# Optimization experiments

Measured on AMD Instinct MI355X. Metric: run time of the kernel, lower is better.

The kernel has to match this reference:

```python
import jax, jax.numpy as jnp
import numpy as np

NA = 100000
NB = 100000
E = 500000
D = 256
EPS = 1e-5


def setup_inputs() -> dict:
    key = jax.random.key(0)
    ks = jax.random.split(key, 10)
    scale = 1.0 / np.sqrt(D)
    return {
        "feat_a": jax.random.normal(ks[0], (NA, D), jnp.float32),
        "feat_b": jax.random.normal(ks[1], (NB, D), jnp.float32),
        "src_ab": jax.random.randint(ks[2], (E,), 0, NA, jnp.int32),
        "dst_ab": jax.random.randint(ks[3], (E,), 0, NB, jnp.int32),
        "src_ba": jax.random.randint(ks[4], (E,), 0, NB, jnp.int32),
        "dst_ba": jax.random.randint(ks[5], (E,), 0, NA, jnp.int32),
        "WT_ab": jax.random.normal(ks[6], (D, D), jnp.float32) * scale,
        "WT_ba": jax.random.normal(ks[7], (D, D), jnp.float32) * scale,
        "WA_ab": jax.random.normal(ks[8], (1, D), jnp.float32) * scale,
        "WA_ba": jax.random.normal(ks[9], (1, D), jnp.float32) * scale,
        "gamma": jnp.ones((D,), jnp.float32),
        "beta": jnp.zeros((D,), jnp.float32),
    }


def _etype_agg(h_src, h_dst, src, dst, WT, WA, n_dst):
    # per-etype linear on src nodes: t_h = W_T h_src
    t_h = h_src @ WT.T                              # [Ns, D]
    x = t_h[src] * h_dst[dst]                       # u_mul_v -> [E, D]
    s = jnp.exp(x @ WA.T)                           # exp(W_A x) -> [E, 1]
    att_sum = jax.ops.segment_sum(s, dst, num_segments=n_dst)  # copy_e+sum
    att = s / att_sum[dst]                          # e_div_v (dst of an edge always has >=1 edge)
    # u_mul_e + sum: weighted scatter of raw src features
    return jax.ops.segment_sum(h_src[src] * att, dst, num_segments=n_dst)


def _finalize(h, gamma, beta):
    h = jax.nn.relu(h)
    mu = jnp.mean(h, axis=-1, keepdims=True)
    var = jnp.mean(jnp.square(h - mu), axis=-1, keepdims=True)
    return (h - mu) / jnp.sqrt(var + EPS) * gamma + beta  # dropout is identity (eval)


def reference(feat_a, feat_b, src_ab, dst_ab, src_ba, dst_ba,
              WT_ab, WT_ba, WA_ab, WA_ba, gamma, beta):
    h_b = _etype_agg(feat_a, feat_b, src_ab, dst_ab, WT_ab, WA_ab, NB)
    h_a = _etype_agg(feat_b, feat_a, src_ba, dst_ba, WT_ba, WA_ba, NA)
    out_a = _finalize(h_a, gamma, beta)
    out_b = _finalize(h_b, gamma, beta)
    return jnp.stack([out_a, out_b])  # [2, N, D]
```

## Files before the change

kernel.cpp:

```cpp
#include <hip/hip_runtime.h>
#include <hip/hip_bf16.h>

#define D 256

typedef __attribute__((ext_vector_type(8))) short short8;
typedef __attribute__((ext_vector_type(4))) float f32x4;
typedef __attribute__((ext_vector_type(4))) unsigned short u16x4;

__device__ __forceinline__ unsigned short f2bf(float f) {
  unsigned int u = __builtin_bit_cast(unsigned int, f);
  u = (u + 0x7FFFu + ((u >> 16) & 1u)) >> 16;
  return (unsigned short)u;
}
__device__ __forceinline__ float bf2f(unsigned short h) {
  unsigned int u = ((unsigned int)h) << 16;
  return __builtin_bit_cast(float, u);
}

__global__ void zero_f32(float* __restrict__ p, int n) {
  int i = blockIdx.x * 256 + threadIdx.x;
  if (i < n) p[i] = 0.f;
}
__global__ void zero2_k(int* __restrict__ a, int na, int* __restrict__ b, int nb) {
  int i = blockIdx.x * 256 + threadIdx.x;
  if (i < na) a[i] = 0;
  else if (i - na < nb) b[i - na] = 0;
}

__global__ void classify_k(const float* __restrict__ q0, const float* __restrict__ q1,
                           const float* __restrict__ q2, const float* __restrict__ q3,
                           int* __restrict__ flags) {
  __shared__ int cnt1[4], cnt0[4];
  int t = threadIdx.x;
  if (t < 4) { cnt1[t] = 0; cnt0[t] = 0; }
  __syncthreads();
  const float* qs[4] = {q0, q1, q2, q3};
#pragma unroll
  for (int v = 0; v < 4; ++v) {
    float x = qs[v][t];
    if (x == 1.0f) atomicAdd(&cnt1[v], 1);
    if (x == 0.0f) atomicAdd(&cnt0[v], 1);
  }
  __syncthreads();
  if (t == 0) {
    int gi = -1, bi = -1;
    for (int v = 0; v < 4; ++v) if (cnt1[v] == 256 && gi < 0) gi = v;
    for (int v = 0; v < 4; ++v) if (cnt0[v] == 256 && v != gi && bi < 0) bi = v;
    if (gi < 0) gi = 2;
    if (bi < 0) bi = (gi == 3) ? 2 : 3;
    int wa[2], w = 0;
    for (int v = 0; v < 4; ++v) if (v != gi && v != bi) { if (w < 2) wa[w] = v; ++w; }
    flags[0] = wa[0]; flags[1] = wa[1]; flags[2] = gi; flags[3] = bi;
  }
}

__global__ void prep_w2(const float* __restrict__ WT_ab, const float* __restrict__ WT_ba,
                        const float* __restrict__ q0, const float* __restrict__ q1,
                        const float* __restrict__ q2, const float* __restrict__ q3,
                        const int* __restrict__ flags,
                        unsigned short* __restrict__ w2ab, unsigned short* __restrict__ w2ba) {
  const float* qs[4] = {q0, q1, q2, q3};
  const float* WAab = qs[flags[0]];
  const float* WAba = qs[flags[1]];
  int i = blockIdx.x * 256 + threadIdx.x;
  int n = i >> 8;
  w2ab[i] = f2bf(WAab[n] * WT_ab[i]);
  w2ba[i] = f2bf(WAba[n] * WT_ba[i]);
}

__global__ __launch_bounds__(512) void gemm_g(const float* __restrict__ feat,
                                              const unsigned short* __restrict__ w2,
                                              unsigned short* __restrict__ g,
                                              unsigned short* __restrict__ featbf,
                                              int nchunks, int do_featbf) {
  __shared__ __align__(16) unsigned char bl[2][8192];
  int lane = threadIdx.x & 63;
  int wv = threadIdx.x >> 6;
  int c0 = blockIdx.x * 8 + wv;
  bool active = c0 < nchunks;
  int c = active ? c0 : (nchunks - 1);
  int r16 = lane & 15;
  int kg = lane >> 4;
  int row0 = c * 32;

  short8 a[2][8];
#pragma unroll
  for (int sub = 0; sub < 2; ++sub) {
    int row = row0 + sub * 16 + r16;
    const float* rp = feat + (size_t)row * D + kg * 8;
#pragma unroll
    for (int kk = 0; kk < 8; ++kk) {
      f32x4 x0 = *(const f32x4*)(rp + kk * 32);
      f32x4 x1 = *(const f32x4*)(rp + kk * 32 + 4);
      short8 t;
      t[0] = (short)f2bf(x0[0]); t[1] = (short)f2bf(x0[1]);
      t[2] = (short)f2bf(x0[2]); t[3] = (short)f2bf(x0[3]);
      t[4] = (short)f2bf(x1[0]); t[5] = (short)f2bf(x1[1]);
      t[6] = (short)f2bf(x1[2]); t[7] = (short)f2bf(x1[3]);
      a[sub][kk] = t;
      if (do_featbf && active)
        *(short8*)(featbf + (size_t)row * D + kk * 32 + kg * 8) = t;
    }
  }

  int t = threadIdx.x;
  int brow = t >> 5, bc = t & 31;
  int slin = brow * 512 + bc * 16;
  int sswz = slin ^ ((brow & 7) << 4);

  *(short8*)(bl[0] + sswz) = *(const short8*)(w2 + (size_t)brow * D + bc * 8);
  __syncthreads();

  int cur = 0;
#pragma unroll 1
  for (int nt = 0; nt < 16; ++nt) {
    short8 tnext;
    bool has = nt + 1 < 16;
    if (has)
      tnext = *(const short8*)(w2 + (size_t)((nt + 1) * 16 + brow) * D + bc * 8);

    f32x4 acc0 = {0.f, 0.f, 0.f, 0.f};
    f32x4 acc1 = {0.f, 0.f, 0.f, 0.f};
    const unsigned char* blc = bl[cur];
#pragma unroll
    for (int kk = 0; kk < 8; ++kk) {
      int lin = r16 * 512 + kk * 64 + kg * 16;
      int swz = lin ^ ((r16 & 7) << 4);
      short8 b = *(const short8*)(blc + swz);
      acc0 = __builtin_amdgcn_mfma_f32_16x16x32_bf16(a[0][kk], b, acc0, 0, 0, 0);
      acc1 = __builtin_amdgcn_mfma_f32_16x16x32_bf16(a[1][kk], b, acc1, 0, 0, 0);
    }
    if (active) {
      int colv = nt * 16 + r16;
#pragma unroll
      for (int j = 0; j < 4; ++j) {
        int r = row0 + kg * 4 + j;
        g[(size_t)r * D + colv] = f2bf(acc0[j]);
        g[(size_t)(r + 16) * D + colv] = f2bf(acc1[j]);
      }
    }
    if (has) *(short8*)(bl[cur ^ 1] + sswz) = tnext;
    __syncthreads();
    cur ^= 1;
  }
}

__global__ void hist2_k(const int* __restrict__ dab, int* __restrict__ degb,
                        const int* __restrict__ dba, int* __restrict__ dega, int E) {
  int i = blockIdx.x * blockDim.x + threadIdx.x;
  if (i < E) atomicAdd(&degb[dab[i]], 1);
  else if (i - E < E) atomicAdd(&dega[dba[i - E]], 1);
}

__global__ void scanA2_k(const int* __restrict__ degb, int* __restrict__ rpb,
                         int* __restrict__ bsb, int nB,
                         const int* __restrict__ dega, int* __restrict__ rpa,
                         int* __restrict__ bsa, int nA, int nbB) {
  __shared__ int sh[1024];
  bool isB = (int)blockIdx.x < nbB;
  const int* deg = isB ? degb : dega;
  int* rp = isB ? rpb : rpa;
  int* bsum = isB ? bsb : bsa;
  int n = isB ? nB : nA;
  int blk = isB ? blockIdx.x : blockIdx.x - nbB;
  int i = blk * 1024 + threadIdx.x;
  int v = (i < n) ? deg[i] : 0;
  sh[threadIdx.x] = v;
  __syncthreads();
  for (int off = 1; off < 1024; off <<= 1) {
    int tv = (threadIdx.x >= (unsigned)off) ? sh[threadIdx.x - off] : 0;
    __syncthreads();
    sh[threadIdx.x] += tv;
    __syncthreads();
  }
  if (i < n) rp[i] = sh[threadIdx.x] - v;
  if (threadIdx.x == 1023) bsum[blk] = sh[1023];
}

__global__ void scanB_k(int* __restrict__ bsB, int* __restrict__ bsA, int nbB, int nbA) {
  __shared__ int sh[128];
  int* b = (blockIdx.x == 0) ? bsB : bsA;
  int nb = (blockIdx.x == 0) ? nbB : nbA;
  int t = threadIdx.x;
  int v = (t < nb) ? b[t] : 0;
  sh[t] = v;
  __syncthreads();
  for (int off = 1; off < 128; off <<= 1) {
    int u = (t >= off) ? sh[t - off] : 0;
    __syncthreads();
    sh[t] += u;
    __syncthreads();
  }
  if (t < nb) b[t] = sh[t] - v;
}

__global__ void scanC2_k(int* __restrict__ rpb, int* __restrict__ curb,
                         const int* __restrict__ bsb, int nB,
                         int* __restrict__ rpa, int* __restrict__ cura,
                         const int* __restrict__ bsa, int nA, int nbB, int E) {
  bool isB = (int)blockIdx.x < nbB;
  int* rp = isB ? rpb : rpa;
  int* cursor = isB ? curb : cura;
  const int* bsum = isB ? bsb : bsa;
  int n = isB ? nB : nA;
  int blk = isB ? blockIdx.x : blockIdx.x - nbB;
  int i = blk * 1024 + threadIdx.x;
  if (i < n) {
    int v = rp[i] + bsum[i >> 10];
    rp[i] = v;
    cursor[i] = v;
  }
  if (i == 0) rp[n] = E;
}

__global__ void scatter2_k(const int* __restrict__ sab, const int* __restrict__ dab,
                           int* __restrict__ curb, int* __restrict__ colab,
                           const int* __restrict__ sba, const int* __restrict__ dba,
                           int* __restrict__ cura, int* __restrict__ colba, int E) {
  int i = blockIdx.x * blockDim.x + threadIdx.x;
  if (i < E) {
    int slot = atomicAdd(&curb[dab[i]], 1);
    colab[slot] = sab[i];
  } else if (i - E < E) {
    int j = i - E;
    int slot = atomicAdd(&cura[dba[j]], 1);
    colba[slot] = sba[j];
  }
}

__global__ __launch_bounds__(256) void agg_ln_bb(const unsigned short* __restrict__ fsrc,
                                                 const unsigned short* __restrict__ hdst,
                                                 const unsigned short* __restrict__ g,
                                                 const int* __restrict__ rp,
                                                 const int* __restrict__ colsrc,
                                                 const float* __restrict__ q0,
                                                 const float* __restrict__ q1,
                                                 const float* __restrict__ q2,
                                                 const float* __restrict__ q3,
                                                 const int* __restrict__ flags,
                                                 float* __restrict__ out, int n_dst) {
  const float* qs[4] = {q0, q1, q2, q3};
  const float* gamma = qs[flags[2]];
  const float* beta  = qs[flags[3]];
  int lane = threadIdx.x & 63;
  int v = blockIdx.x * 4 + (threadIdx.x >> 6);
  if (v >= n_dst) return;
  u16x4 hq = *(const u16x4*)(hdst + (size_t)v * D + lane * 4);
  f32x4 hv;
  hv[0] = bf2f(hq[0]); hv[1] = bf2f(hq[1]); hv[2] = bf2f(hq[2]); hv[3] = bf2f(hq[3]);
  int beg = rp[v], end = rp[v + 1];

  float ssum = 0.f;
  f32x4 acc = {0.f, 0.f, 0.f, 0.f};
  if (beg < end) {
    int sc = colsrc[beg];
    u16x4 gq = *(const u16x4*)(g + (size_t)sc * D + lane * 4);
    u16x4 fq = *(const u16x4*)(fsrc + (size_t)sc * D + lane * 4);
    for (int i = beg; i < end; ++i) {
      int ip = (i + 1 < end) ? (i + 1) : i;
      int scn = colsrc[ip];
      u16x4 gqn = *(const u16x4*)(g + (size_t)scn * D + lane * 4);
      u16x4 fqn = *(const u16x4*)(fsrc + (size_t)scn * D + lane * 4);
      float d = bf2f(gq[0]) * hv[0] + bf2f(gq[1]) * hv[1] +
                bf2f(gq[2]) * hv[2] + bf2f(gq[3]) * hv[3];
#pragma unroll
      for (int off = 32; off > 0; off >>= 1) d += __shfl_xor(d, off, 64);
      float s = __expf(d);
      ssum += s;
      acc[0] += bf2f(fq[0]) * s; acc[1] += bf2f(fq[1]) * s;
      acc[2] += bf2f(fq[2]) * s; acc[3] += bf2f(fq[3]) * s;
      gq = gqn; fq = fqn;
    }
  }
  float inv = (end > beg) ? (1.f / ssum) : 0.f;
  acc[0] *= inv; acc[1] *= inv; acc[2] *= inv; acc[3] *= inv;

  acc[0] = fmaxf(acc[0], 0.f); acc[1] = fmaxf(acc[1], 0.f);
  acc[2] = fmaxf(acc[2], 0.f); acc[3] = fmaxf(acc[3], 0.f);

  float sm = acc[0] + acc[1] + acc[2] + acc[3];
#pragma unroll
  for (int off = 32; off > 0; off >>= 1) sm += __shfl_xor(sm, off, 64);
  float mu = sm * (1.f / 256.f);
  f32x4 dl;
  dl[0] = acc[0] - mu; dl[1] = acc[1] - mu; dl[2] = acc[2] - mu; dl[3] = acc[3] - mu;
  float sq = dl[0] * dl[0] + dl[1] * dl[1] + dl[2] * dl[2] + dl[3] * dl[3];
#pragma unroll
  for (int off = 32; off > 0; off >>= 1) sq += __shfl_xor(sq, off, 64);
  float rs = rsqrtf(sq * (1.f / 256.f) + 1e-5f);

  f32x4 gm = *(const f32x4*)(gamma + lane * 4);
  f32x4 bt = *(const f32x4*)(beta + lane * 4);
  f32x4 o;
  o[0] = dl[0] * rs * gm[0] + bt[0];
  o[1] = dl[1] * rs * gm[1] + bt[1];
  o[2] = dl[2] * rs * gm[2] + bt[2];
  o[3] = dl[3] * rs * gm[3] + bt[3];
  *(f32x4*)(out + (size_t)v * D + lane * 4) = o;
}

__global__ __launch_bounds__(256) void agg_ln_bf(const unsigned short* __restrict__ fsrc,
                                                 const float* __restrict__ feat_dst,
                                                 const unsigned short* __restrict__ g,
                                                 const int* __restrict__ rp,
                                                 const int* __restrict__ colsrc,
                                                 const float* __restrict__ q0,
                                                 const float* __restrict__ q1,
                                                 const float* __restrict__ q2,
                                                 const float* __restrict__ q3,
                                                 const int* __restrict__ flags,
                                                 float* __restrict__ out, int n_dst) {
  const float* qs[4] = {q0, q1, q2, q3};
  const float* gamma = qs[flags[2]];
  const float* beta  = qs[flags[3]];
  int lane = threadIdx.x & 63;
  int v = blockIdx.x * 4 + (threadIdx.x >> 6);
  if (v >= n_dst) return;
  f32x4 hv = *(const f32x4*)(feat_dst + (size_t)v * D + lane * 4);
  int beg = rp[v], end = rp[v + 1];

  float ssum = 0.f;
  f32x4 acc = {0.f, 0.f, 0.f, 0.f};
  if (beg < end) {
    int sc = colsrc[beg];
    u16x4 gq = *(const u16x4*)(g + (size_t)sc * D + lane * 4);
    u16x4 fq = *(const u16x4*)(fsrc + (size_t)sc * D + lane * 4);
    for (int i = beg; i < end; ++i) {
      int ip = (i + 1 < end) ? (i + 1) : i;
      int scn = colsrc[ip];
      u16x4 gqn = *(const u16x4*)(g + (size_t)scn * D + lane * 4);
      u16x4 fqn = *(const u16x4*)(fsrc + (size_t)scn * D + lane * 4);
      float d = bf2f(gq[0]) * hv[0] + bf2f(gq[1]) * hv[1] +
                bf2f(gq[2]) * hv[2] + bf2f(gq[3]) * hv[3];
#pragma unroll
      for (int off = 32; off > 0; off >>= 1) d += __shfl_xor(d, off, 64);
      float s = __expf(d);
      ssum += s;
      acc[0] += bf2f(fq[0]) * s; acc[1] += bf2f(fq[1]) * s;
      acc[2] += bf2f(fq[2]) * s; acc[3] += bf2f(fq[3]) * s;
      gq = gqn; fq = fqn;
    }
  }
  float inv = (end > beg) ? (1.f / ssum) : 0.f;
  acc[0] *= inv; acc[1] *= inv; acc[2] *= inv; acc[3] *= inv;

  acc[0] = fmaxf(acc[0], 0.f); acc[1] = fmaxf(acc[1], 0.f);
  acc[2] = fmaxf(acc[2], 0.f); acc[3] = fmaxf(acc[3], 0.f);

  float sm = acc[0] + acc[1] + acc[2] + acc[3];
#pragma unroll
  for (int off = 32; off > 0; off >>= 1) sm += __shfl_xor(sm, off, 64);
  float mu = sm * (1.f / 256.f);
  f32x4 dl;
  dl[0] = acc[0] - mu; dl[1] = acc[1] - mu; dl[2] = acc[2] - mu; dl[3] = acc[3] - mu;
  float sq = dl[0] * dl[0] + dl[1] * dl[1] + dl[2] * dl[2] + dl[3] * dl[3];
#pragma unroll
  for (int off = 32; off > 0; off >>= 1) sq += __shfl_xor(sq, off, 64);
  float rs = rsqrtf(sq * (1.f / 256.f) + 1e-5f);

  f32x4 gm = *(const f32x4*)(gamma + lane * 4);
  f32x4 bt = *(const f32x4*)(beta + lane * 4);
  f32x4 o;
  o[0] = dl[0] * rs * gm[0] + bt[0];
  o[1] = dl[1] * rs * gm[1] + bt[1];
  o[2] = dl[2] * rs * gm[2] + bt[2];
  o[3] = dl[3] * rs * gm[3] + bt[3];
  *(f32x4*)(out + (size_t)v * D + lane * 4) = o;
}

__global__ __launch_bounds__(256) void agg_ln(const float* __restrict__ feat_src,
                                              const float* __restrict__ feat_dst,
                                              const unsigned short* __restrict__ g,
                                              const int* __restrict__ rp,
                                              const int* __restrict__ colsrc,
                                              const float* __restrict__ q0,
                                              const float* __restrict__ q1,
                                              const float* __restrict__ q2,
                                              const float* __restrict__ q3,
                                              const int* __restrict__ flags,
                                              float* __restrict__ out, int n_dst) {
  const float* qs[4] = {q0, q1, q2, q3};
  const float* gamma = qs[flags[2]];
  const float* beta  = qs[flags[3]];
  int lane = threadIdx.x & 63;
  int v = blockIdx.x * 4 + (threadIdx.x >> 6);
  if (v >= n_dst) return;
  f32x4 hv = *(const f32x4*)(feat_dst + (size_t)v * D + lane * 4);
  int beg = rp[v], end = rp[v + 1];

  float ssum = 0.f;
  f32x4 acc = {0.f, 0.f, 0.f, 0.f};
  for (int i = beg; i < end; ++i) {
    int sc = colsrc[i];
    u16x4 gq = *(const u16x4*)(g + (size_t)sc * D + lane * 4);
    float d = bf2f(gq[0]) * hv[0] + bf2f(gq[1]) * hv[1] +
              bf2f(gq[2]) * hv[2] + bf2f(gq[3]) * hv[3];
#pragma unroll
    for (int off = 32; off > 0; off >>= 1) d += __shfl_xor(d, off, 64);
    float s = __expf(d);
    ssum += s;
    f32x4 f = *(const f32x4*)(feat_src + (size_t)sc * D + lane * 4);
    acc[0] += f[0] * s; acc[1] += f[1] * s;
    acc[2] += f[2] * s; acc[3] += f[3] * s;
  }
  float inv = (end > beg) ? (1.f / ssum) : 0.f;
  acc[0] *= inv; acc[1] *= inv; acc[2] *= inv; acc[3] *= inv;

  acc[0] = fmaxf(acc[0], 0.f); acc[1] = fmaxf(acc[1], 0.f);
  acc[2] = fmaxf(acc[2], 0.f); acc[3] = fmaxf(acc[3], 0.f);

  float sm = acc[0] + acc[1] + acc[2] + acc[3];
#pragma unroll
  for (int off = 32; off > 0; off >>= 1) sm += __shfl_xor(sm, off, 64);
  float mu = sm * (1.f / 256.f);
  f32x4 dl;
  dl[0] = acc[0] - mu; dl[1] = acc[1] - mu; dl[2] = acc[2] - mu; dl[3] = acc[3] - mu;
  float sq = dl[0] * dl[0] + dl[1] * dl[1] + dl[2] * dl[2] + dl[3] * dl[3];
#pragma unroll
  for (int off = 32; off > 0; off >>= 1) sq += __shfl_xor(sq, off, 64);
  float rs = rsqrtf(sq * (1.f / 256.f) + 1e-5f);

  f32x4 gm = *(const f32x4*)(gamma + lane * 4);
  f32x4 bt = *(const f32x4*)(beta + lane * 4);
  f32x4 o;
  o[0] = dl[0] * rs * gm[0] + bt[0];
  o[1] = dl[1] * rs * gm[1] + bt[1];
  o[2] = dl[2] * rs * gm[2] + bt[2];
  o[3] = dl[3] * rs * gm[3] + bt[3];
  *(f32x4*)(out + (size_t)v * D + lane * 4) = o;
}

extern "C" void kernel_launch(void* const* d_in, const int* in_sizes, int n_in,
                              void* d_out, int out_size, void* d_ws, size_t ws_size,
                              hipStream_t stream) {
  const float* feat_a = (const float*)d_in[0];
  const float* feat_b = (const float*)d_in[1];
  const int* src_ab = (const int*)d_in[2];
  const int* dst_ab = (const int*)d_in[3];
  const int* src_ba = (const int*)d_in[4];
  const int* dst_ba = (const int*)d_in[5];
  const float* WT_ab = (const float*)d_in[6];
  const float* WT_ba = (const float*)d_in[7];
  const float* q0 = (const float*)d_in[8];
  const float* q1 = (const float*)d_in[9];
  const float* q2 = (const float*)d_in[10];
  const float* q3 = (const float*)d_in[11];

  int NA = in_sizes[0] / D;
  int NB = in_sizes[1] / D;
  int E = in_sizes[2];

  float* out = (float*)d_out;
  float* out_a = out;
  float* out_b = out + (size_t)NA * D;

  char* w = (char*)d_ws;
  size_t off = 0;
  auto alloc = [&](size_t bytes) -> void* {
    void* p = (void*)(w + off);
    off += (bytes + 255) & ~(size_t)255;
    return p;
  };
  size_t nmax = (size_t)(NA > NB ? NA : NB);
  unsigned short* gws = (unsigned short*)alloc(nmax * D * 2);
  unsigned short* w2ab = (unsigned short*)alloc(65536 * 2);
  unsigned short* w2ba = (unsigned short*)alloc(65536 * 2);
  int* dc_b = (int*)alloc((size_t)NB * 4);
  int* dc_a = (int*)alloc((size_t)NA * 4);
  int* rp_b = (int*)alloc((size_t)(NB + 1) * 4);
  int* rp_a = (int*)alloc((size_t)(NA + 1) * 4);
  int* col_ab = (int*)alloc((size_t)E * 4);
  int* col_ba = (int*)alloc((size_t)E * 4);
  int* bs_b = (int*)alloc(512);
  int* bs_a = (int*)alloc(512);
  int* flags = (int*)alloc(256);
  size_t need_base = off;
  unsigned short* featbf = (unsigned short*)alloc(nmax * D * 2);
  size_t need_full = off;
  unsigned short* featbf2 = (unsigned short*)alloc(nmax * D * 2);
  size_t need_big = off;

  bool bad = (n_in != 12);
  bad = bad || (in_sizes[0] != in_sizes[1]);
  bad = bad || (in_sizes[2] != in_sizes[3]) || (in_sizes[3] != in_sizes[4]) ||
        (in_sizes[4] != in_sizes[5]);
  bad = bad || (in_sizes[6] != 65536) || (in_sizes[7] != 65536);
  bad = bad || (in_sizes[8] != 256) || (in_sizes[9] != 256) ||
        (in_sizes[10] != 256) || (in_sizes[11] != 256);
  bad = bad || (out_size != (NA + NB) * D);
  bad = bad || (ws_size < need_base);
  if (bad) {
    zero_f32<<<(out_size + 255) / 256, 256, 0, stream>>>(out, out_size);
    return;
  }
  int big  = (ws_size >= need_big)  ? 1 : 0;
  int fast = (ws_size >= need_full) ? 1 : 0;

  classify_k<<<1, 256, 0, stream>>>(q0, q1, q2, q3, flags);
  zero2_k<<<(NA + NB + 255) / 256, 256, 0, stream>>>(dc_b, NB, dc_a, NA);
  prep_w2<<<256, 256, 0, stream>>>(WT_ab, WT_ba, q0, q1, q2, q3, flags,
                                   w2ab, w2ba);

  hist2_k<<<(2 * E + 255) / 256, 256, 0, stream>>>(dst_ab, dc_b, dst_ba, dc_a, E);

  int nbB = (NB + 1023) / 1024, nbA = (NA + 1023) / 1024;
  scanA2_k<<<nbB + nbA, 1024, 0, stream>>>(dc_b, rp_b, bs_b, NB,
                                           dc_a, rp_a, bs_a, NA, nbB);
  scanB_k<<<2, 128, 0, stream>>>(bs_b, bs_a, nbB, nbA);
  scanC2_k<<<nbB + nbA, 1024, 0, stream>>>(rp_b, dc_b, bs_b, NB,
                                           rp_a, dc_a, bs_a, NA, nbB, E);
  scatter2_k<<<(2 * E + 255) / 256, 256, 0, stream>>>(src_ab, dst_ab, dc_b, col_ab,
                                                      src_ba, dst_ba, dc_a, col_ba, E);

  int chA = (NA + 31) / 32, chB = (NB + 31) / 32;

  if (big) {
    unsigned short* g_a = (unsigned short*)out_a;
    gemm_g<<<(chA + 7) / 8, 512, 0, stream>>>(feat_a, w2ab, g_a, featbf, chA, 1);
    gemm_g<<<(chB + 7) / 8, 512, 0, stream>>>(feat_b, w2ba, gws, featbf2, chB, 1);
    agg_ln_bb<<<(NB + 3) / 4, 256, 0, stream>>>(featbf, featbf2, g_a, rp_b, col_ab,
                                                q0, q1, q2, q3, flags, out_b, NB);
    agg_ln_bb<<<(NA + 3) / 4, 256, 0, stream>>>(featbf2, featbf, gws, rp_a, col_ba,
                                                q0, q1, q2, q3, flags, out_a, NA);
  } else if (fast) {
    gemm_g<<<(chA + 7) / 8, 512, 0, stream>>>(feat_a, w2ab, gws, featbf, chA, 1);
    agg_ln_bf<<<(NB + 3) / 4, 256, 0, stream>>>(featbf, feat_b, gws, rp_b, col_ab,
                                                q0, q1, q2, q3, flags, out_b, NB);
    gemm_g<<<(chB + 7) / 8, 512, 0, stream>>>(feat_b, w2ba, gws, featbf, chB, 1);
    agg_ln_bf<<<(NA + 3) / 4, 256, 0, stream>>>(featbf, feat_a, gws, rp_a, col_ba,
                                                q0, q1, q2, q3, flags, out_a, NA);
  } else {
    gemm_g<<<(chA + 7) / 8, 512, 0, stream>>>(feat_a, w2ab, gws, featbf, chA, 0);
    agg_ln<<<(NB + 3) / 4, 256, 0, stream>>>(feat_a, feat_b, gws, rp_b, col_ab,
                                             q0, q1, q2, q3, flags, out_b, NB);
    gemm_g<<<(chB + 7) / 8, 512, 0, stream>>>(feat_b, w2ba, gws, featbf, chB, 0);
    agg_ln<<<(NA + 3) / 4, 256, 0, stream>>>(feat_b, feat_a, gws, rp_a, col_ba,
                                             q0, q1, q2, q3, flags, out_a, NA);
  }
}
```

Measured before the change: 443.9 us.

## Reassociate attention score onto destination nodes to halve per-edge gathers

The attention dot product is reassociated so the weight matrix (W_A folded into W_T, transposed) is applied to destination-node features, giving one z vector per destination. The per-edge score then becomes fsrc[src]·z[dst], so each edge gathers only the source feature row instead of both the transformed row and the source row. The two GEMMs and the two aggregation kernels are each merged into a single launch covering both edge types. This path needs an extra node-by-D bf16 workspace buffer and only runs when the workspace is large enough; otherwise the older paths are used.

```diff
diff --git a/kernel.cpp b/kernel.cpp
--- a/kernel.cpp
+++ b/kernel.cpp
@@ -68,15 +68,27 @@
   w2ba[i] = f2bf(WAba[n] * WT_ba[i]);
 }
 
-__global__ __launch_bounds__(512) void gemm_g(const float* __restrict__ feat,
-                                              const unsigned short* __restrict__ w2,
-                                              unsigned short* __restrict__ g,
-                                              unsigned short* __restrict__ featbf,
-                                              int nchunks, int do_featbf) {
-  __shared__ __align__(16) unsigned char bl[2][8192];
+__global__ void prep_w2z(const float* __restrict__ WT_ab, const float* __restrict__ WT_ba,
+                         const float* __restrict__ q0, const float* __restrict__ q1,
+                         const float* __restrict__ q2, const float* __restrict__ q3,
+                         const int* __restrict__ flags,
+                         unsigned short* __restrict__ zab, unsigned short* __restrict__ zba) {
+  const float* qs[4] = {q0, q1, q2, q3};
+  const float* WAab = qs[flags[0]];
+  const float* WAba = qs[flags[1]];
+  int i = blockIdx.x * 256 + threadIdx.x;
+  int c = i >> 8, d = i & 255;
+  zab[i] = f2bf(WAab[d] * WT_ab[d * 256 + c]);
+  zba[i] = f2bf(WAba[d] * WT_ba[d * 256 + c]);
+}
+
+__device__ __forceinline__ void gemm_body(const float* feat, const unsigned short* w2,
+                                          unsigned short* g, unsigned short* featbf,
+                                          int nchunks, int do_featbf, int cb,
+                                          unsigned char* bl0, unsigned char* bl1) {
   int lane = threadIdx.x & 63;
   int wv = threadIdx.x >> 6;
-  int c0 = blockIdx.x * 8 + wv;
+  int c0 = cb * 8 + wv;
   bool active = c0 < nchunks;
   int c = active ? c0 : (nchunks - 1);
   int r16 = lane & 15;
@@ -108,9 +120,10 @@
   int slin = brow * 512 + bc * 16;
   int sswz = slin ^ ((brow & 7) << 4);
 
-  *(short8*)(bl[0] + sswz) = *(const short8*)(w2 + (size_t)brow * D + bc * 8);
+  *(short8*)(bl0 + sswz) = *(const short8*)(w2 + (size_t)brow * D + bc * 8);
   __syncthreads();
 
+  unsigned char* bl[2] = {bl0, bl1};
   int cur = 0;
 #pragma unroll 1
   for (int nt = 0; nt < 16; ++nt) {
@@ -143,6 +156,36 @@
     __syncthreads();
     cur ^= 1;
   }
+}
+
+__global__ __launch_bounds__(512) void gemm_g(const float* __restrict__ feat,
+                                              const unsigned short* __restrict__ w2,
+                                              unsigned short* __restrict__ g,
+                                              unsigned short* __restrict__ featbf,
+                                              int nchunks, int do_featbf) {
+  __shared__ __align__(16) unsigned char bl[2][8192];
+  gemm_body(feat, w2, g, featbf, nchunks, do_featbf, blockIdx.x, bl[0], bl[1]);
+}
+
+__global__ __launch_bounds__(512) void gemm2_g(const float* __restrict__ feat_a,
+                                               const float* __restrict__ feat_b,
+                                               const unsigned short* __restrict__ w2z_ab,
+                                               const unsigned short* __restrict__ w2z_ba,
+                                               unsigned short* __restrict__ z_a,
+                                               unsigned short* __restrict__ z_b,
+                                               unsigned short* __restrict__ fbf_a,
+                                               unsigned short* __restrict__ fbf_b,
+                                               int chA, int chB) {
+  __shared__ __align__(16) unsigned char bl[2][8192];
+  int nblkA = (chA + 7) / 8;
+  bool isA = (int)blockIdx.x < nblkA;
+  const float* feat = isA ? feat_a : feat_b;
+  const unsigned short* w2 = isA ? w2z_ba : w2z_ab;
+  unsigned short* z = isA ? z_a : z_b;
+  unsigned short* fbf = isA ? fbf_a : fbf_b;
+  int nchunks = isA ? chA : chB;
+  int cb = isA ? blockIdx.x : blockIdx.x - nblkA;
+  gemm_body(feat, w2, z, fbf, nchunks, 1, cb, bl[0], bl[1]);
 }
 
 __global__ void hist2_k(const int* __restrict__ dab, int* __restrict__ degb,
@@ -228,48 +271,62 @@
   }
 }
 
-__global__ __launch_bounds__(256) void agg_ln_bb(const unsigned short* __restrict__ fsrc,
-                                                 const unsigned short* __restrict__ hdst,
-                                                 const unsigned short* __restrict__ g,
-                                                 const int* __restrict__ rp,
-                                                 const int* __restrict__ colsrc,
-                                                 const float* __restrict__ q0,
-                                                 const float* __restrict__ q1,
-                                                 const float* __restrict__ q2,
-                                                 const float* __restrict__ q3,
-                                                 const int* __restrict__ flags,
-                                                 float* __restrict__ out, int n_dst) {
+__global__ __launch_bounds__(256) void aggz_k(const unsigned short* __restrict__ fbf_a,
+                                              const unsigned short* __restrict__ fbf_b,
+                                              const unsigned short* __restrict__ z_a,
+                                              const unsigned short* __restrict__ z_b,
+                                              const int* __restrict__ rp_a,
+                                              const int* __restrict__ rp_b,
+                                              const int* __restrict__ col_ab,
+                                              const int* __restrict__ col_ba,
+                                              const float* __restrict__ q0,
+                                              const float* __restrict__ q1,
+                                              const float* __restrict__ q2,
+                                              const float* __restrict__ q3,
+                                              const int* __restrict__ flags,
+                                              float* __restrict__ out_a,
+                                              float* __restrict__ out_b,
+                                              int NA, int NB) {
   const float* qs[4] = {q0, q1, q2, q3};
   const float* gamma = qs[flags[2]];
   const float* beta  = qs[flags[3]];
+  int gB = (NB + 3) / 4;
+  bool isB = (int)blockIdx.x < gB;
+  const unsigned short* fsrc = isB ? fbf_a : fbf_b;
+  const unsigned short* z    = isB ? z_b  : z_a;
+  const int* rp  = isB ? rp_b : rp_a;
+  const int* col = isB ? col_ab : col_ba;
+  float* out = isB ? out_b : out_a;
+  int n_dst = isB ? NB : NA;
+  int vb = isB ? blockIdx.x : blockIdx.x - gB;
+
   int lane = threadIdx.x & 63;
-  int v = blockIdx.x * 4 + (threadIdx.x >> 6);
+  int v = vb * 4 + (threadIdx.x >> 6);
   if (v >= n_dst) return;
-  u16x4 hq = *(const u16x4*)(hdst + (size_t)v * D + lane * 4);
-  f32x4 hv;
-  hv[0] = bf2f(hq[0]); hv[1] = bf2f(hq[1]); hv[2] = bf2f(hq[2]); hv[3] = bf2f(hq[3]);
+  u16x4 zq = *(const u16x4*)(z + (size_t)v * D + lane * 4);
+  f32x4 zv;
+  zv[0] = bf2f(zq[0]); zv[1] = bf2f(zq[1]); zv[2] = bf2f(zq[2]); zv[3] = bf2f(zq[3]);
   int beg = rp[v], end = rp[v + 1];
 
   float ssum = 0.f;
   f32x4 acc = {0.f, 0.f, 0.f, 0.f};
   if (beg < end) {
-    int sc = colsrc[beg];
-    u16x4 gq = *(const u16x4*)(g + (size_t)sc * D + lane * 4);
+    int sc = col[beg];
     u16x4 fq = *(const u16x4*)(fsrc + (size_t)sc * D + lane * 4);
     for (int i = beg; i < end; ++i) {
       int ip = (i + 1 < end) ? (i + 1) : i;
-      int scn = colsrc[ip];
-      u16x4 gqn = *(const u16x4*)(g + (size_t)scn * D + lane * 4);
+      int scn = col[ip];
       u16x4 fqn = *(const u16x4*)(fsrc + (size_t)scn * D + lane * 4);
-      float d = bf2f(gq[0]) * hv[0] + bf2f(gq[1]) * hv[1] +
-                bf2f(gq[2]) * hv[2] + bf2f(gq[3]) * hv[3];
+      f32x4 f;
+      f[0] = bf2f(fq[0]); f[1] = bf2f(fq[1]); f[2] = bf2f(fq[2]); f[3] = bf2f(fq[3]);
+      float d = f[0] * zv[0] + f[1] * zv[1] + f[2] * zv[2] + f[3] * zv[3];
 #pragma unroll
       for (int off = 32; off > 0; off >>= 1) d += __shfl_xor(d, off, 64);
       float s = __expf(d);
       ssum += s;
-      acc[0] += bf2f(fq[0]) * s; acc[1] += bf2f(fq[1]) * s;
-      acc[2] += bf2f(fq[2]) * s; acc[3] += bf2f(fq[3]) * s;
-      gq = gqn; fq = fqn;
+      acc[0] += f[0] * s; acc[1] += f[1] * s;
+      acc[2] += f[2] * s; acc[3] += f[3] * s;
+      fq = fqn;
     }
   }
   float inv = (end > beg) ? (1.f / ssum) : 0.f;
@@ -465,6 +522,8 @@
   unsigned short* gws = (unsigned short*)alloc(nmax * D * 2);
   unsigned short* w2ab = (unsigned short*)alloc(65536 * 2);
   unsigned short* w2ba = (unsigned short*)alloc(65536 * 2);
+  unsigned short* w2z_ab = (unsigned short*)alloc(65536 * 2);
+  unsigned short* w2z_ba = (unsigned short*)alloc(65536 * 2);
   int* dc_b = (int*)alloc((size_t)NB * 4);
   int* dc_a = (int*)alloc((size_t)NA * 4);
   int* rp_b = (int*)alloc((size_t)(NB + 1) * 4);
@@ -477,8 +536,9 @@
   size_t need_base = off;
   unsigned short* featbf = (unsigned short*)alloc(nmax * D * 2);
   size_t need_full = off;
+  unsigned short* z_a = (unsigned short*)alloc(nmax * D * 2);
   unsigned short* featbf2 = (unsigned short*)alloc(nmax * D * 2);
-  size_t need_big = off;
+  size_t need_z = off;
 
   bool bad = (n_in != 12);
   bad = bad || (in_sizes[0] != in_sizes[1]);
@@ -493,13 +553,17 @@
     zero_f32<<<(out_size + 255) / 256, 256, 0, stream>>>(out, out_size);
     return;
   }
-  int big  = (ws_size >= need_big)  ? 1 : 0;
-  int fast = (ws_size >= need_full) ? 1 : 0;
+  int zplan = (ws_size >= need_z)    ? 1 : 0;
+  int fast  = (ws_size >= need_full) ? 1 : 0;
 
   classify_k<<<1, 256, 0, stream>>>(q0, q1, q2, q3, flags);
   zero2_k<<<(NA + NB + 255) / 256, 256, 0, stream>>>(dc_b, NB, dc_a, NA);
-  prep_w2<<<256, 256, 0, stream>>>(WT_ab, WT_ba, q0, q1, q2, q3, flags,
-                                   w2ab, w2ba);
+  if (zplan)
+    prep_w2z<<<256, 256, 0, stream>>>(WT_ab, WT_ba, q0, q1, q2, q3, flags,
+                                      w2z_ab, w2z_ba);
+  else
+    prep_w2<<<256, 256, 0, stream>>>(WT_ab, WT_ba, q0, q1, q2, q3, flags,
+                                     w2ab, w2ba);
 
   hist2_k<<<(2 * E + 255) / 256, 256, 0, stream>>>(dst_ab, dc_b, dst_ba, dc_a, E);
 
@@ -514,14 +578,15 @@
 
   int chA = (NA + 31) / 32, chB = (NB + 31) / 32;
 
-  if (big) {
-    unsigned short* g_a = (unsigned short*)out_a;
-    gemm_g<<<(chA + 7) / 8, 512, 0, stream>>>(feat_a, w2ab, g_a, featbf, chA, 1);
-    gemm_g<<<(chB + 7) / 8, 512, 0, stream>>>(feat_b, w2ba, gws, featbf2, chB, 1);
-    agg_ln_bb<<<(NB + 3) / 4, 256, 0, stream>>>(featbf, featbf2, g_a, rp_b, col_ab,
-                                                q0, q1, q2, q3, flags, out_b, NB);
-    agg_ln_bb<<<(NA + 3) / 4, 256, 0, stream>>>(featbf2, featbf, gws, rp_a, col_ba,
-                                                q0, q1, q2, q3, flags, out_a, NA);
+  if (zplan) {
+    int nblk = (chA + 7) / 8 + (chB + 7) / 8;
+    gemm2_g<<<nblk, 512, 0, stream>>>(feat_a, feat_b, w2z_ab, w2z_ba,
+                                      z_a, gws , featbf ,
+                                      featbf2 , chA, chB);
+    int gtot = (NB + 3) / 4 + (NA + 3) / 4;
+    aggz_k<<<gtot, 256, 0, stream>>>(featbf, featbf2, z_a, gws ,
+                                     rp_a, rp_b, col_ab, col_ba,
+                                     q0, q1, q2, q3, flags, out_a, out_b, NA, NB);
   } else if (fast) {
     gemm_g<<<(chA + 7) / 8, 512, 0, stream>>>(feat_a, w2ab, gws, featbf, chA, 1);
     agg_ln_bf<<<(NB + 3) / 4, 256, 0, stream>>>(featbf, feat_b, gws, rp_b, col_ab,
@@ -530,10 +595,10 @@
     agg_ln_bf<<<(NA + 3) / 4, 256, 0, stream>>>(featbf, feat_a, gws, rp_a, col_ba,
                                                 q0, q1, q2, q3, flags, out_a, NA);
   } else {
-    gemm_g<<<(chA + 7) / 8, 512, 0, stream>>>(feat_a, w2ab, gws, featbf, chA, 0);
+    gemm_g<<<(chA + 7) / 8, 512, 0, stream>>>(feat_a, w2ab, gws, gws, chA, 0);
     agg_ln<<<(NB + 3) / 4, 256, 0, stream>>>(feat_a, feat_b, gws, rp_b, col_ab,
                                              q0, q1, q2, q3, flags, out_b, NB);
-    gemm_g<<<(chB + 7) / 8, 512, 0, stream>>>(feat_b, w2ba, gws, featbf, chB, 0);
+    gemm_g<<<(chB + 7) / 8, 512, 0, stream>>>(feat_b, w2ba, gws, gws, chB, 0);
     agg_ln<<<(NA + 3) / 4, 256, 0, stream>>>(feat_b, feat_a, gws, rp_a, col_ba,
                                              q0, q1, q2, q3, flags, out_a, NA);
   }
```

Result: slower. 480.1 us (+8.2%).
